# Kernel optimization log

Hardware: AMD Instinct MI355X
Metric: run time of the kernel (lower is better)

## Reference

```python
import jax, jax.numpy as jnp
import numpy as np

B, IN, CTX, OUT = 4096, 256, 64, 128
N, K, J = 128, 4, 64            # n_neurons, n_branches, branch_size (both layers)
NG = N * K                      # gates per layer = 512
WS = IN * NG                    # gating weight count per layer (gating always sees original x)
TP = 2 * (WS + NG)              # total hypernetwork output params = 263168
S = 0.05


def setup_inputs() -> dict:
    key = jax.random.key(0)
    ks = jax.random.split(key, 20)
    r = lambda i, shape: jax.random.normal(ks[i], shape, dtype=jnp.float32) * S
    return {
        "x": jax.random.normal(ks[0], (B, IN), dtype=jnp.float32),
        "context": jax.random.normal(ks[1], (CTX,), dtype=jnp.float32),
        # layer 0 (in=256): per-neuron per-branch linear + soma
        "Wb0": r(2, (N, K, J, IN)), "bb0": r(3, (N, K, J)),
        "Ws0": r(4, (N, K * J)),    "bs0": r(5, (N,)),
        # layer 1 (in=128)
        "Wb1": r(6, (N, K, J, N)),  "bb1": r(7, (N, K, J)),
        "Ws1": r(8, (N, K * J)),    "bs1": r(9, (N,)),
        # output layer
        "Wout": r(10, (OUT, N)), "bout": r(11, (OUT,)),
        # hypernetwork: ctx -> 32 -> 64 -> TP
        "h1w": r(12, (32, CTX)), "h1b": r(13, (32,)),
        "h2w": r(14, (64, 32)),  "h2b": r(15, (64,)),
        "h3w": r(16, (TP, 64)),  "h3b": r(17, (TP,)),
    }


def _dann_layer(cur, x, gw_slice, Wb, bb, Ws, bs):
    # gating weights derived from hypernetwork output vector (shared across batch)
    Wg = gw_slice[:WS].reshape(NG, IN)
    bg = gw_slice[WS:WS + NG]
    gates = jax.nn.sigmoid(x @ Wg.T + bg).reshape(-1, N, K, 1)      # [B,N,K,1]
    h = jax.nn.relu(jnp.einsum('bi,nkji->bnkj', cur, Wb) + bb) * gates
    return jnp.einsum('bnkj,nkj->bn', h, Ws.reshape(N, K, J)) + bs  # [B,N]


def reference(x, context, Wb0, bb0, Ws0, bs0, Wb1, bb1, Ws1, bs1,
              Wout, bout, h1w, h1b, h2w, h2b, h3w, h3b):
    # hypernetwork (dropout inactive at inference); single context -> one weight vector
    hv = jax.nn.relu(context @ h1w.T + h1b)
    hv = jax.nn.relu(hv @ h2w.T + h2b)
    gw = hv @ h3w.T + h3b                                           # [TP]
    per = WS + NG
    cur = _dann_layer(x,   x, gw[:per],        Wb0, bb0, Ws0, bs0)
    cur = _dann_layer(cur, x, gw[per:2 * per], Wb1, bb1, Ws1, bs1)
    return cur @ Wout.T + bout
```

## Files before the change

### kernel.cpp

```cpp
#include <hip/hip_runtime.h>

#define BB   4096
#define IN_  256
#define NN   128
#define NG   512
#define WS_  131072
#define PER  131584
#define TP   263168

typedef __attribute__((ext_vector_type(8))) short short8;
typedef __attribute__((ext_vector_type(4))) float f32x4;

#define VW(N) asm volatile("s_waitcnt vmcnt(" #N ")" ::: "memory")

__device__ __forceinline__ unsigned short f2bf(float f){
  unsigned u = __float_as_uint(f);
  return (unsigned short)((u + 0x7fffu + ((u >> 16) & 1u)) >> 16);
}

__device__ __forceinline__ void gload16(const void* g, void* l){
  __builtin_amdgcn_global_load_lds((const __attribute__((address_space(1))) void*)g,
                                   (__attribute__((address_space(3))) void*)l, 16, 0, 0);
}

__device__ __forceinline__ float rowred16(float s){
  s += __int_as_float(__builtin_amdgcn_update_dpp(0, __float_as_int(s), 0xB1,  0xF, 0xF, true));
  s += __int_as_float(__builtin_amdgcn_update_dpp(0, __float_as_int(s), 0x4E,  0xF, 0xF, true));
  s += __int_as_float(__builtin_amdgcn_update_dpp(0, __float_as_int(s), 0x124, 0xF, 0xF, true));
  s += __int_as_float(__builtin_amdgcn_update_dpp(0, __float_as_int(s), 0x128, 0xF, 0xF, true));
  return s;
}

__global__ void k_convert(const float* __restrict__ x, unsigned short* __restrict__ xb){
  size_t i = ((size_t)blockIdx.x*256 + threadIdx.x)*4;
  float4 v = *(const float4*)(x + i);
  ushort4 o;
  o.x = f2bf(v.x); o.y = f2bf(v.y); o.z = f2bf(v.z); o.w = f2bf(v.w);
  *(ushort4*)(xb + i) = o;
}

__global__ __launch_bounds__(512)
void k_gw(const float* __restrict__ ctx,
          const float* __restrict__ h1w, const float* __restrict__ h1b,
          const float* __restrict__ h2w, const float* __restrict__ h2b,
          const float* __restrict__ h3w, const float* __restrict__ h3b,
          unsigned short* __restrict__ Wg_bf, float* __restrict__ bg){
  __shared__ float s1[32];
  __shared__ float hv2[64];
  const int t = threadIdx.x;
  if (t < 32){
    float a = h1b[t];
    #pragma unroll 8
    for (int i = 0; i < 64; ++i) a += ctx[i]*h1w[t*64+i];
    s1[t] = fmaxf(a, 0.f);
  }
  __syncthreads();
  if (t < 64){
    float a = h2b[t];
    #pragma unroll 8
    for (int i = 0; i < 32; ++i) a += s1[i]*h2w[t*32+i];
    hv2[t] = fmaxf(a, 0.f);
  }
  __syncthreads();

  const int r = blockIdx.x*64 + (t >> 3);
  const int q = t & 7;
  const float4* row = (const float4*)(h3w + (size_t)r*64);
  float4 v0 = row[q*2], v1 = row[q*2+1];
  float4 h0 = *(const float4*)(hv2 + q*8), h1 = *(const float4*)(hv2 + q*8 + 4);
  float a = v0.x*h0.x + v0.y*h0.y + v0.z*h0.z + v0.w*h0.w
          + v1.x*h1.x + v1.y*h1.y + v1.z*h1.z + v1.w*h1.w;
  a += __shfl_xor(a, 1);
  a += __shfl_xor(a, 2);
  a += __shfl_xor(a, 4);
  if (q == 0){
    a += h3b[r];
    if (r < WS_)          Wg_bf[r] = f2bf(a);
    else if (r < PER)     bg[r - WS_] = a;
    else if (r < PER+WS_) Wg_bf[WS_ + (r - PER)] = f2bf(a);
    else                  bg[512 + (r - (PER+WS_))] = a;
  }
}

__global__ __launch_bounds__(512, 1)
void k_gates(const unsigned short* __restrict__ Wg_bf,
             const unsigned short* __restrict__ x_bf,
             const float* __restrict__ bg,
             float* __restrict__ GT){
  __shared__ __align__(16) unsigned short As[128*64];
  __shared__ __align__(16) unsigned short Bs[256*64];
  const int tid  = threadIdx.x;
  const int lane = tid & 63;
  const int wid  = tid >> 6;
  const int wm = wid >> 2, wn = wid & 3;
  const int lrow = lane & 15, lk = lane >> 4;
  const int m0 = blockIdx.x*128;
  const int b0 = blockIdx.y*256;

  f32x4 zero = {0.f,0.f,0.f,0.f};
  f32x4 acc[4][4];
  #pragma unroll
  for (int i=0;i<4;++i)
    #pragma unroll
    for (int j=0;j<4;++j) acc[i][j] = zero;

  for (int kt = 0; kt < 256/64; ++kt){
    __syncthreads();
    #pragma unroll
    for (int i = 0; i < 2; ++i){
      int c = tid + i*512;
      int row = c >> 3, k8 = c & 7;
      uint4 v = *(const uint4*)(Wg_bf + (size_t)(m0+row)*256 + kt*64 + k8*8);
      int idx = (row*64 + k8*8) ^ ((row & 7) << 3);
      *(uint4*)(&As[idx]) = v;
    }
    #pragma unroll
    for (int i = 0; i < 4; ++i){
      int c = tid + i*512;
      int row = c >> 3, k8 = c & 7;
      uint4 v = *(const uint4*)(x_bf + (size_t)(b0+row)*256 + kt*64 + k8*8);
      int idx = (row*64 + k8*8) ^ ((row & 7) << 3);
      *(uint4*)(&Bs[idx]) = v;
    }
    __syncthreads();
    #pragma unroll
    for (int kk = 0; kk < 2; ++kk){
      short8 a[4], b[4];
      #pragma unroll
      for (int fm = 0; fm < 4; ++fm){
        int m = wm*64 + fm*16 + lrow;
        int idx = (m*64 + kk*32 + lk*8) ^ ((m & 7) << 3);
        a[fm] = *(const short8*)(&As[idx]);
      }
      #pragma unroll
      for (int fn = 0; fn < 4; ++fn){
        int r = wn*64 + fn*16 + lrow;
        int idx = (r*64 + kk*32 + lk*8) ^ ((r & 7) << 3);
        b[fn] = *(const short8*)(&Bs[idx]);
      }
      #pragma unroll
      for (int fm = 0; fm < 4; ++fm)
        #pragma unroll
        for (int fn = 0; fn < 4; ++fn)
          acc[fm][fn] = __builtin_amdgcn_mfma_f32_16x16x32_bf16(a[fm], b[fn], acc[fm][fn], 0, 0, 0);
    }
  }
  #pragma unroll
  for (int fm = 0; fm < 4; ++fm){
    float4 bgv = *(const float4*)(bg + m0 + wm*64 + fm*16 + lk*4);
    float bga[4] = {bgv.x, bgv.y, bgv.z, bgv.w};
    #pragma unroll
    for (int reg = 0; reg < 4; ++reg){
      int m = m0 + wm*64 + fm*16 + lk*4 + reg;
      #pragma unroll
      for (int fn = 0; fn < 4; ++fn){
        int b = b0 + wn*64 + fn*16 + lrow;
        float z = acc[fm][fn][reg] + bga[reg];
        GT[(size_t)m*4096 + b] = 1.f/(1.f + __expf(-z));
      }
    }
  }
}

template<int KIN, int LAYER>
__global__ __launch_bounds__(1024, 1)
void k_layer(const unsigned short* __restrict__ Abf,
             const float* __restrict__ Wf32,
             const float* __restrict__ bb,
             const float* __restrict__ Ws,
             const float* __restrict__ GT,
             float* __restrict__ partg){
  constexpr int NT     = KIN/64;
  constexpr int SC     = (LAYER==0) ? 128 : 256;
  constexpr int WN     = SC/64;
  constexpr int BTR    = (LAYER==0) ? 256 : 128;
  constexpr int NBT    = 16;
  constexpr int NPH    = NBT*NT;
  constexpr int AI     = BTR/128;
  constexpr int ABUFS  = BTR*64;
  constexpr unsigned ABYTES = ABUFS*2;
  constexpr int WBOFFS = 2*ABUFS;
  constexpr unsigned WBYTES = WBOFFS*2;
  constexpr unsigned KTB = SC*64*2;
  __shared__ __align__(16) unsigned short lds[WBOFFS + SC*64*NT];

  const int tid  = threadIdx.x;
  const int lane = tid & 63;
  const int wid  = tid >> 6;
  const int wn   = wid % WN, wm = wid / WN;
  const int lrow = lane & 15, lk = lane >> 4;

  const int id      = blockIdx.x;
  const int n       = id >> 1;
  const int sub     = id & 1;
  const int kgrp    = (LAYER==0) ? sub*2 + wn : wn;
  const int abase   = (LAYER==0) ? 0 : sub*2048;
  const int colbase = n*256 + ((LAYER==0) ? sub*128 : 0);

  f32x4 zero = {0.f,0.f,0.f,0.f};
  f32x4 acc[2][4];
  #pragma unroll
  for (int i=0;i<2;++i)
    #pragma unroll
    for (int jj=0;jj<4;++jj) acc[i][jj] = zero;

  auto STAGE_A = [&](int buf, int bt, int kt){
    #pragma unroll
    for (int i = 0; i < AI; ++i){
      int c = i*1024 + tid;
      int r = c >> 3, kc = c & 7;
      const unsigned short* s = Abf + (size_t)(abase + bt*BTR + r)*KIN + kt*64 + ((kc ^ (r&7))<<3);
      gload16(s, &lds[buf*ABUFS + (i*1024 + wid*64)*8]);
    }
  };

  STAGE_A(0, 0, 0);
  asm volatile("" ::: "memory");
  {
    constexpr int CHPR = KIN/8;
    float4 va[4], vb[4];
    #pragma unroll
    for (int j = 0; j < 4; ++j){
      int c = j*1024 + tid;
      int r = c / CHPR, q = c % CHPR;
      const float4* s = (const float4*)(Wf32 + (size_t)(colbase + r)*KIN + q*8);
      va[j] = s[0]; vb[j] = s[1];
    }
    #pragma unroll
    for (int j = 0; j < 4; ++j){
      int c = j*1024 + tid;
      int r = c / CHPR, q = c % CHPR;
      int kt = q >> 3, k8 = q & 7;
      short8 p;
      p[0] = (short)f2bf(va[j].x); p[1] = (short)f2bf(va[j].y);
      p[2] = (short)f2bf(va[j].z); p[3] = (short)f2bf(va[j].w);
      p[4] = (short)f2bf(vb[j].x); p[5] = (short)f2bf(vb[j].y);
      p[6] = (short)f2bf(vb[j].z); p[7] = (short)f2bf(vb[j].w);
      int dst = WBOFFS + kt*SC*64 + ((r*64 + k8*8) ^ ((r&7)<<3));
      *(short8*)(&lds[dst]) = p;
    }
  }
  asm volatile("s_waitcnt lgkmcnt(0)" ::: "memory");

  float bbv[4], wsv[4];
  #pragma unroll
  for (int fn = 0; fn < 4; ++fn){
    int cloc = ((LAYER==0) ? sub*128 : 0) + wn*64 + fn*16 + lrow;
    bbv[fn] = bb[n*256 + cloc];
    wsv[fn] = Ws[n*256 + cloc];
  }
  const float* gtrow = GT + (size_t)(LAYER*512 + n*4 + kgrp)*4096 + abase;
  float* prow = partg + (size_t)kgrp*524288 + (size_t)n*4096 + abase;

  unsigned aoff[2], boff[4];
  #pragma unroll
  for (int fm = 0; fm < 2; ++fm){
    int m = wm*32 + fm*16 + lrow;
    aoff[fm] = 2u*((unsigned)((m*64 + lk*8) ^ ((m & 7) << 3)));
  }
  #pragma unroll
  for (int fn = 0; fn < 4; ++fn){
    int r = wn*64 + fn*16 + lrow;
    boff[fn] = 2u*((unsigned)((r*64 + lk*8) ^ ((r & 7) << 3)));
  }
  const char* ldsc = (const char*)lds;
  unsigned abufB = 0;

  #pragma unroll 1
  for (int bt = 0; bt < NBT; ++bt){
    float4 gv[2];
    #pragma unroll
    for (int kt = 0; kt < NT; ++kt){
      const int  ph  = bt*NT + kt;
      const bool epi = (kt == NT-1);

      if (ph == 0)                VW(0);
      else if (NT == 2)           VW(2);
      else if (kt <= 1)           VW(2);
      else                        VW(0);
      __builtin_amdgcn_s_barrier();

      if (ph + 1 < NPH){
        int bt2 = bt, kt2 = kt + 1;
        if (kt2 == NT){ kt2 = 0; bt2 = bt + 1; }
        STAGE_A(abufB ? 0 : 1, bt2, kt2);
      }
      asm volatile("" ::: "memory");

      if (kt == 0){
        #pragma unroll
        for (int fm = 0; fm < 2; ++fm)
          gv[fm] = *(const float4*)(gtrow + bt*BTR + wm*32 + fm*16 + lk*4);
        asm volatile("" ::: "memory");
      }

      #pragma unroll
      for (int kk = 0; kk < 2; ++kk){
        short8 a[2], b[4];
        #pragma unroll
        for (int fm = 0; fm < 2; ++fm)
          a[fm] = *(const short8*)(ldsc + (abufB + (aoff[fm] ^ (unsigned)(kk*64))));
        #pragma unroll
        for (int fn = 0; fn < 4; ++fn)
          b[fn] = *(const short8*)(ldsc + WBYTES + kt*KTB + (boff[fn] ^ (unsigned)(kk*64)));
        #pragma unroll
        for (int fm = 0; fm < 2; ++fm)
          #pragma unroll
          for (int fn = 0; fn < 4; ++fn)
            acc[fm][fn] = __builtin_amdgcn_mfma_f32_16x16x32_bf16(a[fm], b[fn], acc[fm][fn], 0, 0, 0);
      }

      if (epi){
        #pragma unroll
        for (int fm = 0; fm < 2; ++fm){
          float gr[4] = {gv[fm].x, gv[fm].y, gv[fm].z, gv[fm].w};
          float sums[4];
          #pragma unroll
          for (int reg = 0; reg < 4; ++reg){
            float s = 0.f;
            #pragma unroll
            for (int fn = 0; fn < 4; ++fn)
              s += fmaxf(acc[fm][fn][reg] + bbv[fn], 0.f) * wsv[fn];
            sums[reg] = rowred16(s * gr[reg]);
          }
          if (lrow == 0){
            float4 o; o.x = sums[0]; o.y = sums[1]; o.z = sums[2]; o.w = sums[3];
            *(float4*)(prow + bt*BTR + wm*32 + fm*16 + lk*4) = o;
          }
        }
        #pragma unroll
        for (int i2 = 0; i2 < 2; ++i2)
          #pragma unroll
          for (int j2 = 0; j2 < 4; ++j2) acc[i2][j2] = zero;
      }
      abufB ^= ABYTES;
    }
  }
}

template<int OUT_BF>
__global__ void k_mid(const float* __restrict__ partg, const float* __restrict__ bsv,
                      unsigned short* __restrict__ obf, float* __restrict__ of32){
  const int n = blockIdx.x;
  const int t = threadIdx.x;
  const float* p = partg + (size_t)n*4096 + t*16;
  const float bsn = bsv[n];
  #pragma unroll
  for (int i = 0; i < 4; ++i){
    float4 s0 = *(const float4*)(p + i*4);
    float4 s1 = *(const float4*)(p + 524288 + i*4);
    float4 s2 = *(const float4*)(p + 2*524288 + i*4);
    float4 s3 = *(const float4*)(p + 3*524288 + i*4);
    float v0 = ((s0.x + s1.x) + s2.x) + s3.x + bsn;
    float v1 = ((s0.y + s1.y) + s2.y) + s3.y + bsn;
    float v2 = ((s0.z + s1.z) + s2.z) + s3.z + bsn;
    float v3 = ((s0.w + s1.w) + s2.w) + s3.w + bsn;
    size_t b = (size_t)t*16 + i*4;
    if (OUT_BF){
      obf[(b+0)*128 + n] = f2bf(v0);
      obf[(b+1)*128 + n] = f2bf(v1);
      obf[(b+2)*128 + n] = f2bf(v2);
      obf[(b+3)*128 + n] = f2bf(v3);
    } else {
      of32[(b+0)*128 + n] = v0;
      of32[(b+1)*128 + n] = v1;
      of32[(b+2)*128 + n] = v2;
      of32[(b+3)*128 + n] = v3;
    }
  }
}

__global__ void k_final(const float* __restrict__ out1, const float* __restrict__ Wout,
                        const float* __restrict__ bout, float* __restrict__ out){
  int t = blockIdx.x*256 + threadIdx.x;
  int b = t >> 7, o = t & 127;
  const float4* cr = (const float4*)(out1 + (size_t)b*128);
  const float4* wr = (const float4*)(Wout + (size_t)o*128);
  float a = 0.f;
  #pragma unroll
  for (int i = 0; i < 32; ++i){
    float4 c = cr[i], w = wr[i];
    a += c.x*w.x + c.y*w.y + c.z*w.z + c.w*w.w;
  }
  out[t] = a + bout[o];
}

extern "C" void kernel_launch(void* const* d_in, const int* in_sizes, int n_in,
                              void* d_out, int out_size, void* d_ws, size_t ws_size,
                              hipStream_t stream){
  const float* x    = (const float*)d_in[0];
  const float* ctx  = (const float*)d_in[1];
  const float* Wb0  = (const float*)d_in[2];
  const float* bb0  = (const float*)d_in[3];
  const float* Ws0  = (const float*)d_in[4];
  const float* bs0  = (const float*)d_in[5];
  const float* Wb1  = (const float*)d_in[6];
  const float* bb1  = (const float*)d_in[7];
  const float* Ws1  = (const float*)d_in[8];
  const float* bs1  = (const float*)d_in[9];
  const float* Wout = (const float*)d_in[10];
  const float* bout = (const float*)d_in[11];
  const float* h1w  = (const float*)d_in[12];
  const float* h1b  = (const float*)d_in[13];
  const float* h2w  = (const float*)d_in[14];
  const float* h2b  = (const float*)d_in[15];
  const float* h3w  = (const float*)d_in[16];
  const float* h3b  = (const float*)d_in[17];
  float* out = (float*)d_out;

  char* ws = (char*)d_ws;
  size_t o = 0;
  unsigned short* x_bf  = (unsigned short*)(ws + o); o += (size_t)4096*256*2;
  unsigned short* Wg_bf = (unsigned short*)(ws + o); o += (size_t)1024*256*2;
  float* bg     = (float*)(ws + o); o += 1024*4;
  float* GT     = (float*)(ws + o); o += (size_t)1024*4096*4;
  unsigned short* cur_bf = (unsigned short*)(ws + o); o += (size_t)4096*128*2;
  float* out1   = (float*)(ws + o); o += (size_t)4096*128*4;
  float* partg0 = (float*)(ws + o); o += (size_t)4*128*4096*4;
  float* partg1 = (float*)(ws + o); o += (size_t)4*128*4096*4;

  k_convert<<<1024, 256, 0, stream>>>(x, x_bf);
  k_gw<<<4112, 512, 0, stream>>>(ctx, h1w, h1b, h2w, h2b, h3w, h3b, Wg_bf, bg);
  k_gates<<<dim3(8, 16), 512, 0, stream>>>(Wg_bf, x_bf, bg, GT);
  k_layer<256, 0><<<256, 1024, 0, stream>>>(x_bf, Wb0, bb0, Ws0, GT, partg0);
  k_mid<1><<<128, 256, 0, stream>>>(partg0, bs0, cur_bf, nullptr);
  k_layer<128, 1><<<256, 1024, 0, stream>>>(cur_bf, Wb1, bb1, Ws1, GT, partg1);
  k_mid<0><<<128, 256, 0, stream>>>(partg1, bs1, nullptr, out1);
  k_final<<<2048, 256, 0, stream>>>(out1, Wout, bout, out);
}
```

Before: 211.7 us.

## Load activation fragments directly to registers instead of staging through LDS

Replaces the double-buffered global-to-LDS staging of the bf16 activation tiles with direct per-lane global loads into a two-deep register buffer, prefetching the next phase while the current one feeds MFMA. This removes the per-phase barriers and vmcnt waits plus the LDS traffic for A, and keeps LDS only for the bf16 weights. In exchange, the waves sharing a batch tile (the WN column waves) each fetch the same rows from global memory, relying on cache hits, and register pressure rises.

```diff
diff --git a/kernel.cpp b/kernel.cpp
--- a/kernel.cpp
+++ b/kernel.cpp
@@ -11,16 +11,9 @@
 typedef __attribute__((ext_vector_type(8))) short short8;
 typedef __attribute__((ext_vector_type(4))) float f32x4;
 
-#define VW(N) asm volatile("s_waitcnt vmcnt(" #N ")" ::: "memory")
-
 __device__ __forceinline__ unsigned short f2bf(float f){
   unsigned u = __float_as_uint(f);
   return (unsigned short)((u + 0x7fffu + ((u >> 16) & 1u)) >> 16);
-}
-
-__device__ __forceinline__ void gload16(const void* g, void* l){
-  __builtin_amdgcn_global_load_lds((const __attribute__((address_space(1))) void*)g,
-                                   (__attribute__((address_space(3))) void*)l, 16, 0, 0);
 }
 
 __device__ __forceinline__ float rowred16(float s){
@@ -170,19 +163,14 @@
              const float* __restrict__ Ws,
              const float* __restrict__ GT,
              float* __restrict__ partg){
-  constexpr int NT     = KIN/64;
-  constexpr int SC     = (LAYER==0) ? 128 : 256;
-  constexpr int WN     = SC/64;
-  constexpr int BTR    = (LAYER==0) ? 256 : 128;
-  constexpr int NBT    = 16;
-  constexpr int NPH    = NBT*NT;
-  constexpr int AI     = BTR/128;
-  constexpr int ABUFS  = BTR*64;
-  constexpr unsigned ABYTES = ABUFS*2;
-  constexpr int WBOFFS = 2*ABUFS;
-  constexpr unsigned WBYTES = WBOFFS*2;
+  constexpr int NT   = KIN/64;
+  constexpr int SC   = (LAYER==0) ? 128 : 256;
+  constexpr int WN   = SC/64;
+  constexpr int BTR  = (LAYER==0) ? 256 : 128;
+  constexpr int NBT  = 16;
+  constexpr int NPH  = NBT*NT;
   constexpr unsigned KTB = SC*64*2;
-  __shared__ __align__(16) unsigned short lds[WBOFFS + SC*64*NT];
+  __shared__ __align__(16) unsigned short lds[SC*64*NT];
 
   const int tid  = threadIdx.x;
   const int lane = tid & 63;
@@ -204,18 +192,6 @@
     #pragma unroll
     for (int jj=0;jj<4;++jj) acc[i][jj] = zero;
 
-  auto STAGE_A = [&](int buf, int bt, int kt){
-    #pragma unroll
-    for (int i = 0; i < AI; ++i){
-      int c = i*1024 + tid;
-      int r = c >> 3, kc = c & 7;
-      const unsigned short* s = Abf + (size_t)(abase + bt*BTR + r)*KIN + kt*64 + ((kc ^ (r&7))<<3);
-      gload16(s, &lds[buf*ABUFS + (i*1024 + wid*64)*8]);
-    }
-  };
-
-  STAGE_A(0, 0, 0);
-  asm volatile("" ::: "memory");
   {
     constexpr int CHPR = KIN/8;
     float4 va[4], vb[4];
@@ -236,11 +212,24 @@
       p[2] = (short)f2bf(va[j].z); p[3] = (short)f2bf(va[j].w);
       p[4] = (short)f2bf(vb[j].x); p[5] = (short)f2bf(vb[j].y);
       p[6] = (short)f2bf(vb[j].z); p[7] = (short)f2bf(vb[j].w);
-      int dst = WBOFFS + kt*SC*64 + ((r*64 + k8*8) ^ ((r&7)<<3));
+      int dst = kt*SC*64 + ((r*64 + k8*8) ^ ((r&7)<<3));
       *(short8*)(&lds[dst]) = p;
     }
   }
-  asm volatile("s_waitcnt lgkmcnt(0)" ::: "memory");
+
+  const unsigned short* abp = Abf + (size_t)(abase + wm*32 + lrow)*KIN + lk*8;
+
+  short8 areg[2][2][2];
+  #define ALOAD(BUF, BT, KT)                                                   \
+    _Pragma("unroll")                                                          \
+    for (int kk_ = 0; kk_ < 2; ++kk_)                                          \
+      _Pragma("unroll")                                                        \
+      for (int fm_ = 0; fm_ < 2; ++fm_)                                        \
+        areg[BUF][kk_][fm_] = *(const short8*)(abp +                           \
+            (size_t)((BT)*BTR + fm_*16)*KIN + (KT)*64 + kk_*32);
+
+  ALOAD(0, 0, 0)
+  __syncthreads();
 
   float bbv[4], wsv[4];
   #pragma unroll
@@ -252,65 +241,48 @@
   const float* gtrow = GT + (size_t)(LAYER*512 + n*4 + kgrp)*4096 + abase;
   float* prow = partg + (size_t)kgrp*524288 + (size_t)n*4096 + abase;
 
-  unsigned aoff[2], boff[4];
-  #pragma unroll
-  for (int fm = 0; fm < 2; ++fm){
-    int m = wm*32 + fm*16 + lrow;
-    aoff[fm] = 2u*((unsigned)((m*64 + lk*8) ^ ((m & 7) << 3)));
-  }
+  unsigned boff[4];
   #pragma unroll
   for (int fn = 0; fn < 4; ++fn){
     int r = wn*64 + fn*16 + lrow;
     boff[fn] = 2u*((unsigned)((r*64 + lk*8) ^ ((r & 7) << 3)));
   }
   const char* ldsc = (const char*)lds;
-  unsigned abufB = 0;
 
   #pragma unroll 1
   for (int bt = 0; bt < NBT; ++bt){
     float4 gv[2];
     #pragma unroll
     for (int kt = 0; kt < NT; ++kt){
-      const int  ph  = bt*NT + kt;
-      const bool epi = (kt == NT-1);
-
-      if (ph == 0)                VW(0);
-      else if (NT == 2)           VW(2);
-      else if (kt <= 1)           VW(2);
-      else                        VW(0);
-      __builtin_amdgcn_s_barrier();
+      const int ph = bt*NT + kt;
+      const int cb = kt & 1;
 
       if (ph + 1 < NPH){
-        int bt2 = bt, kt2 = kt + 1;
-        if (kt2 == NT){ kt2 = 0; bt2 = bt + 1; }
-        STAGE_A(abufB ? 0 : 1, bt2, kt2);
-      }
-      asm volatile("" ::: "memory");
-
+        int bt2 = (kt == NT-1) ? bt+1 : bt;
+        int kt2 = (kt == NT-1) ? 0    : kt+1;
+        if (cb == 0) { ALOAD(1, bt2, kt2) }
+        else         { ALOAD(0, bt2, kt2) }
+      }
       if (kt == 0){
-        #pragma unroll
-        for (int fm = 0; fm < 2; ++fm)
-          gv[fm] = *(const float4*)(gtrow + bt*BTR + wm*32 + fm*16 + lk*4);
-        asm volatile("" ::: "memory");
+        gv[0] = *(const float4*)(gtrow + bt*BTR + wm*32 + lk*4);
+        gv[1] = *(const float4*)(gtrow + bt*BTR + wm*32 + 16 + lk*4);
       }
 
       #pragma unroll
       for (int kk = 0; kk < 2; ++kk){
-        short8 a[2], b[4];
-        #pragma unroll
-        for (int fm = 0; fm < 2; ++fm)
-          a[fm] = *(const short8*)(ldsc + (abufB + (aoff[fm] ^ (unsigned)(kk*64))));
+        short8 b[4];
         #pragma unroll
         for (int fn = 0; fn < 4; ++fn)
-          b[fn] = *(const short8*)(ldsc + WBYTES + kt*KTB + (boff[fn] ^ (unsigned)(kk*64)));
+          b[fn] = *(const short8*)(ldsc + kt*KTB + (boff[fn] ^ (unsigned)(kk*64)));
         #pragma unroll
         for (int fm = 0; fm < 2; ++fm)
           #pragma unroll
           for (int fn = 0; fn < 4; ++fn)
-            acc[fm][fn] = __builtin_amdgcn_mfma_f32_16x16x32_bf16(a[fm], b[fn], acc[fm][fn], 0, 0, 0);
-      }
-
-      if (epi){
+            acc[fm][fn] = __builtin_amdgcn_mfma_f32_16x16x32_bf16(
+                areg[cb][kk][fm], b[fn], acc[fm][fn], 0, 0, 0);
+      }
+
+      if (kt == NT-1){
         #pragma unroll
         for (int fm = 0; fm < 2; ++fm){
           float gr[4] = {gv[fm].x, gv[fm].y, gv[fm].z, gv[fm].w};
@@ -333,9 +305,9 @@
           #pragma unroll
           for (int j2 = 0; j2 < 4; ++j2) acc[i2][j2] = zero;
       }
-      abufB ^= ABYTES;
-    }
-  }
+    }
+  }
+  #undef ALOAD
 }
 
 template<int OUT_BF>
```

New measurement: 630.8 us. 198% more time.
